# Optimization experiments

Measured on AMD Instinct MI355X. Metric: run time of the kernel, lower is better.

The kernel has to match this reference:

```python
import jax, jax.numpy as jnp
import numpy as np

N = 50000      # nodes
E = 800000     # edges (before self-loops)
IN = 64        # in_dim
C = 64         # hidden_dim (per-head out channels)
H = 4          # heads
NEG_SLOPE = 0.2


def setup_inputs() -> dict:
    key = jax.random.key(0)
    ks = jax.random.split(key, 9)
    x = jax.random.normal(ks[0], (N, IN), jnp.float32)
    edge_index = jax.random.randint(ks[1], (2, E), 0, N)
    edge_attr = jax.random.uniform(ks[2], (E, 1), jnp.float32)
    s_in = 1.0 / np.sqrt(IN)
    s_c = 1.0 / np.sqrt(C)
    W = jax.random.normal(ks[3], (IN, H * C), jnp.float32) * s_in
    att_src = jax.random.normal(ks[4], (H, C), jnp.float32) * s_c
    att_dst = jax.random.normal(ks[5], (H, C), jnp.float32) * s_c
    lin_edge_w = jax.random.normal(ks[6], (1, H * C), jnp.float32)
    att_edge = jax.random.normal(ks[7], (H, C), jnp.float32) * s_c
    bias = jnp.zeros((C,), jnp.float32)
    return dict(x=x, edge_index=edge_index, edge_attr=edge_attr, W=W,
                att_src=att_src, att_dst=att_dst, lin_edge_w=lin_edge_w,
                att_edge=att_edge, bias=bias)


def reference(x, edge_index, edge_attr, W, att_src, att_dst, lin_edge_w, att_edge, bias):
    n = x.shape[0]
    # add self-loops (PyG default add_self_loops=True, fill_value='mean')
    loop = jnp.arange(n)
    src = jnp.concatenate([edge_index[0], loop])          # [E+N]
    dst = jnp.concatenate([edge_index[1], loop])          # [E+N]
    ea = jnp.concatenate([edge_attr,
                          jnp.full((n, 1), edge_attr.mean(), edge_attr.dtype)], axis=0)
    # node transform: [N, H, C]
    h = (x @ W).reshape(n, H, C)
    a_src = jnp.einsum('nhc,hc->nh', h, att_src)          # [N, H]
    a_dst = jnp.einsum('nhc,hc->nh', h, att_dst)          # [N, H]
    eh = (ea @ lin_edge_w).reshape(-1, H, C)              # [E+N, H, C]
    a_edge = jnp.einsum('ehc,hc->eh', eh, att_edge)       # [E+N, H]
    # per-edge attention logit
    alpha = a_src[src] + a_dst[dst] + a_edge              # [E+N, H]
    alpha = jax.nn.leaky_relu(alpha, NEG_SLOPE)
    # segment softmax over edges grouped by destination node
    amax = jax.ops.segment_max(alpha, dst, num_segments=n)
    alpha = jnp.exp(alpha - amax[dst])
    asum = jax.ops.segment_sum(alpha, dst, num_segments=n)
    alpha = alpha / (asum[dst] + 1e-16)                   # [E+N, H]
    # weighted message + scatter-add aggregation
    msg = h[src] * alpha[..., None]                       # [E+N, H, C]
    out = jax.ops.segment_sum(msg, dst, num_segments=n)   # [N, H, C]
    out = out.mean(axis=1) + bias                         # concat=False -> head mean
    # ReLU + residual
    return jax.nn.relu(out) + x
```

## Files before the change

### kernel.cpp

```cpp
#include <hip/hip_runtime.h>
#include <hip/hip_fp16.h>
#include <math.h>

#define H 4
#define C 64
#define HC 256
#define NEG 0.2f
#define ROWU 64
#define MAXREC 63
#define XPAD 72
#define HPAD 264
#define BKT 128
#define BSH 7
#define TILE 2048
#define SEG 32
#define SEGSH 5

typedef __attribute__((ext_vector_type(8))) _Float16 half8;
typedef __attribute__((ext_vector_type(4))) float f32x4;
typedef float f32x2 __attribute__((vector_size(8)));

__global__ __launch_bounds__(256) void phase1_kernel(
    const float* __restrict__ x, const float* __restrict__ W,
    const float* __restrict__ att_src, const float* __restrict__ att_dst,
    const int* __restrict__ ei, const float* __restrict__ edge_attr,
    unsigned char* __restrict__ h, float* __restrict__ a_src, float* __restrict__ a_dst,
    uint2* __restrict__ arena, unsigned* __restrict__ counts,
    float* __restrict__ mean_acc, int Nn, int Ee, int G1, int ntile) {
    int t = threadIdx.x;
    if ((int)blockIdx.x < G1) {
        __shared__ __align__(16) _Float16 xs[16 * XPAD];
        __shared__ __align__(16) _Float16 hs[16 * HPAD];
        int w = t >> 6, lane = t & 63, quad = lane >> 4, c16 = lane & 15;
        half8 bf[4][2];
#pragma unroll
        for (int nt = 0; nt < 4; ++nt)
#pragma unroll
            for (int kh = 0; kh < 2; ++kh)
#pragma unroll
                for (int j = 0; j < 8; ++j)
                    bf[nt][kh][j] = (_Float16)W[(kh * 32 + quad * 8 + j) * HC +
                                                w * 64 + nt * 16 + c16];
        float ats[4], atd[4];
#pragma unroll
        for (int nt = 0; nt < 4; ++nt) {
            ats[nt] = att_src[w * 64 + nt * 16 + c16];
            atd[nt] = att_dst[w * 64 + nt * 16 + c16];
        }

        int nTiles = (Nn + 15) >> 4;
        for (int mt = blockIdx.x; mt < nTiles; mt += G1) {
            __syncthreads();
            {
                int row = t >> 4, col4 = (t & 15) * 4;
                int node = mt * 16 + row;
                float4 v = make_float4(0.f, 0.f, 0.f, 0.f);
                if (node < Nn) v = *(const float4*)(x + (size_t)node * 64 + col4);
                _Float16* dst = xs + row * XPAD + col4;
                dst[0] = (_Float16)v.x; dst[1] = (_Float16)v.y;
                dst[2] = (_Float16)v.z; dst[3] = (_Float16)v.w;
            }
            __syncthreads();
            half8 a0 = *(const half8*)(xs + c16 * XPAD + quad * 8);
            half8 a1 = *(const half8*)(xs + c16 * XPAD + 32 + quad * 8);
            f32x4 d[4];
#pragma unroll
            for (int nt = 0; nt < 4; ++nt) {
                f32x4 acc = {0.f, 0.f, 0.f, 0.f};
                acc = __builtin_amdgcn_mfma_f32_16x16x32_f16(a0, bf[nt][0], acc, 0, 0, 0);
                acc = __builtin_amdgcn_mfma_f32_16x16x32_f16(a1, bf[nt][1], acc, 0, 0, 0);
                d[nt] = acc;
            }
#pragma unroll
            for (int reg = 0; reg < 4; ++reg) {
                float ps = 0.f, pd = 0.f;
#pragma unroll
                for (int nt = 0; nt < 4; ++nt) {
                    ps += d[nt][reg] * ats[nt];
                    pd += d[nt][reg] * atd[nt];
                }
                ps += __shfl_xor(ps, 1); pd += __shfl_xor(pd, 1);
                ps += __shfl_xor(ps, 2); pd += __shfl_xor(pd, 2);
                ps += __shfl_xor(ps, 4); pd += __shfl_xor(pd, 4);
                ps += __shfl_xor(ps, 8); pd += __shfl_xor(pd, 8);
                if (c16 == 0) {
                    int node = mt * 16 + quad * 4 + reg;
                    if (node < Nn) {
                        a_src[node * 4 + w] = ps;
                        a_dst[node * 4 + w] = pd;
                    }
                }
            }
#pragma unroll
            for (int nt = 0; nt < 4; ++nt)
#pragma unroll
                for (int reg = 0; reg < 4; ++reg)
                    hs[(quad * 4 + reg) * HPAD + w * 64 + nt * 16 + c16] =
                        (_Float16)d[nt][reg];
            __syncthreads();
            {
                int row = t >> 4, chunk = t & 15;
                int node = mt * 16 + row;
                if (node < Nn) {
                    const uint4* sp = (const uint4*)(hs + row * HPAD + chunk * 16);
                    uint4 sA = sp[0], sB = sp[1];
                    unsigned ua[8] = {sA.x, sA.y, sA.z, sA.w, sB.x, sB.y, sB.z, sB.w};
                    unsigned ow[4];
#pragma unroll
                    for (int q = 0; q < 4; ++q) {
                        float2 p0 = __half22float2(*reinterpret_cast<const __half2*>(&ua[q * 2]));
                        float2 p1 = __half22float2(*reinterpret_cast<const __half2*>(&ua[q * 2 + 1]));
                        int v = __builtin_amdgcn_cvt_pk_fp8_f32(p0.x, p0.y, 0, false);
                        v = __builtin_amdgcn_cvt_pk_fp8_f32(p1.x, p1.y, v, true);
                        ow[q] = (unsigned)v;
                    }
                    *(uint4*)(h + (size_t)node * HC + chunk * 16) =
                        make_uint4(ow[0], ow[1], ow[2], ow[3]);
                }
            }
        }
    } else {
        __shared__ float red[256];
        __shared__ unsigned cntA[512];
        int nbkt = (Nn + BKT - 1) >> BSH;
        int tile = (int)blockIdx.x - G1;
        for (int bb = t; bb < nbkt; bb += 256) cntA[bb] = 0;
        __syncthreads();
        int e0 = tile * TILE;
        float s = 0.f;
#pragma unroll 4
        for (int k = 0; k < TILE / 256; ++k) {
            int i = e0 + k * 256 + t;
            if (i < Ee) {
                int src = ei[i];
                int dst = ei[Ee + i];
                float ea = edge_attr[i];
                s += ea;
                unsigned q = (unsigned)(ea * 65535.f + 0.5f);
                int b = dst >> BSH;
                unsigned r = atomicAdd(&cntA[b], 1u);
                if (r < SEG)
                    arena[((size_t)b * ntile + tile) * SEG + r] =
                        make_uint2((q << 16) | (unsigned)src,
                                   (unsigned)(dst & (BKT - 1)));
            }
        }
        __syncthreads();
        for (int bb = t; bb < nbkt; bb += 256) {
            unsigned c = cntA[bb];
            counts[(size_t)bb * ntile + tile] = c < (unsigned)SEG ? c : (unsigned)SEG;
        }
        red[t] = s;
        __syncthreads();
        for (int o = 128; o; o >>= 1) {
            if (t < o) red[t] += red[t + o];
            __syncthreads();
        }
        if (t == 0) atomicAdd(mean_acc, red[0]);
    }
}

__global__ __launch_bounds__(256) void bucket_kernel(
    const uint2* __restrict__ arena, const unsigned* __restrict__ counts,
    unsigned* __restrict__ edges, int ntile) {
    __shared__ unsigned rows[BKT * ROWU];
    __shared__ unsigned cnt[BKT];
    __shared__ unsigned short segc[512];
    int b = blockIdx.x, t = threadIdx.x;
    if (t < BKT) cnt[t] = 0;
    for (int j = t; j < ntile; j += 256)
        segc[j] = (unsigned short)counts[(size_t)b * ntile + j];
    __syncthreads();
    int total = ntile * SEG;
    size_t base = (size_t)b * ntile * SEG;
    for (int j = t; j < total; j += 256) {
        int seg = j >> SEGSH, slot = j & (SEG - 1);
        if (slot < (int)segc[seg]) {
            uint2 e = arena[base + j];
            unsigned r = atomicAdd(&cnt[e.y], 1u);
            if (r < MAXREC) rows[e.y * ROWU + 1 + r] = e.x;
        }
    }
    __syncthreads();
    if (t < BKT) rows[t * ROWU] = cnt[t] < (unsigned)MAXREC ? cnt[t] : (unsigned)MAXREC;
    __syncthreads();
    size_t obase = (size_t)b * (BKT * ROWU);
    for (int i = t; i < BKT * (ROWU / 4); i += 256)
        *(uint4*)(edges + obase + i * 4) = *(const uint4*)(rows + i * 4);
}

__global__ __launch_bounds__(256) void aggregate_kernel(
    const unsigned* __restrict__ edges,
    const float* __restrict__ a_src, const float* __restrict__ a_dst,
    const float* __restrict__ lin_edge_w, const float* __restrict__ att_edge,
    const float* __restrict__ mean_acc, const unsigned char* __restrict__ h,
    const float* __restrict__ bias, const float* __restrict__ x,
    float* __restrict__ out, int Nn, float invE) {
    int lane = threadIdx.x & 63;
    int n = blockIdx.x * 4 + (threadIdx.x >> 6);
    if (n >= Nn) return;
    int head = lane >> 4;

    size_t rowbase = (size_t)n * ROWU;
    unsigned deg = edges[rowbase];
    unsigned rec = edges[rowbase + 1 + lane];
    const unsigned* h8 = (const unsigned*)h;
    unsigned sv = h8[(size_t)n * 64 + lane];
    float mean = mean_acc[0] * invE;
    float ad = a_dst[n * 4 + head];
    float asn = a_src[n * 4 + head];

    int sub = lane & 15;
    float kp = 0.f;
#pragma unroll
    for (int j = 0; j < 4; ++j) {
        int c = sub * 4 + j;
        kp += lin_edge_w[head * C + c] * att_edge[head * C + c];
    }
    kp += __shfl_xor(kp, 1);
    kp += __shfl_xor(kp, 2);
    kp += __shfl_xor(kp, 4);
    kp += __shfl_xor(kp, 8);
    float K = kp;
    const float DEQ = 1.0f / 65535.f;

    if (deg > MAXREC) deg = MAXREC;

    float ls = asn + ad + mean * K;
    ls = ls > 0.f ? ls : NEG * ls;
    float wsl = __expf(ls);
    f32x2 s01 = __builtin_amdgcn_cvt_pk_f32_fp8((int)sv, false);
    f32x2 s23 = __builtin_amdgcn_cvt_pk_f32_fp8((int)sv, true);
    float4 acc = make_float4(wsl * s01[0], wsl * s01[1], wsl * s23[0], wsl * s23[1]);
    float swgt = wsl;

    int i = 0;
    for (; i + 4 <= (int)deg; i += 4) {
        unsigned r0 = (unsigned)__builtin_amdgcn_readlane((int)rec, i + 0);
        unsigned r1 = (unsigned)__builtin_amdgcn_readlane((int)rec, i + 1);
        unsigned r2 = (unsigned)__builtin_amdgcn_readlane((int)rec, i + 2);
        unsigned r3 = (unsigned)__builtin_amdgcn_readlane((int)rec, i + 3);
        int s0 = r0 & 0xFFFF, s1 = r1 & 0xFFFF, s2 = r2 & 0xFFFF, s3 = r3 & 0xFFFF;
        unsigned hv0 = h8[(size_t)s0 * 64 + lane];
        unsigned hv1 = h8[(size_t)s1 * 64 + lane];
        unsigned hv2 = h8[(size_t)s2 * 64 + lane];
        unsigned hv3 = h8[(size_t)s3 * 64 + lane];
        float l0 = a_src[s0 * 4 + head] + ad + (float)(r0 >> 16) * DEQ * K;
        float l1 = a_src[s1 * 4 + head] + ad + (float)(r1 >> 16) * DEQ * K;
        float l2 = a_src[s2 * 4 + head] + ad + (float)(r2 >> 16) * DEQ * K;
        float l3 = a_src[s3 * 4 + head] + ad + (float)(r3 >> 16) * DEQ * K;
        l0 = l0 > 0.f ? l0 : NEG * l0;
        l1 = l1 > 0.f ? l1 : NEG * l1;
        l2 = l2 > 0.f ? l2 : NEG * l2;
        l3 = l3 > 0.f ? l3 : NEG * l3;
        float w0 = __expf(l0), w1 = __expf(l1), w2 = __expf(l2), w3 = __expf(l3);
        swgt += (w0 + w1) + (w2 + w3);
        {
            f32x2 f01 = __builtin_amdgcn_cvt_pk_f32_fp8((int)hv0, false);
            f32x2 f23 = __builtin_amdgcn_cvt_pk_f32_fp8((int)hv0, true);
            acc.x += w0 * f01[0]; acc.y += w0 * f01[1];
            acc.z += w0 * f23[0]; acc.w += w0 * f23[1];
        }
        {
            f32x2 f01 = __builtin_amdgcn_cvt_pk_f32_fp8((int)hv1, false);
            f32x2 f23 = __builtin_amdgcn_cvt_pk_f32_fp8((int)hv1, true);
            acc.x += w1 * f01[0]; acc.y += w1 * f01[1];
            acc.z += w1 * f23[0]; acc.w += w1 * f23[1];
        }
        {
            f32x2 f01 = __builtin_amdgcn_cvt_pk_f32_fp8((int)hv2, false);
            f32x2 f23 = __builtin_amdgcn_cvt_pk_f32_fp8((int)hv2, true);
            acc.x += w2 * f01[0]; acc.y += w2 * f01[1];
            acc.z += w2 * f23[0]; acc.w += w2 * f23[1];
        }
        {
            f32x2 f01 = __builtin_amdgcn_cvt_pk_f32_fp8((int)hv3, false);
            f32x2 f23 = __builtin_amdgcn_cvt_pk_f32_fp8((int)hv3, true);
            acc.x += w3 * f01[0]; acc.y += w3 * f01[1];
            acc.z += w3 * f23[0]; acc.w += w3 * f23[1];
        }
    }
    for (; i < (int)deg; ++i) {
        unsigned r = (unsigned)__builtin_amdgcn_readlane((int)rec, i);
        int s0 = r & 0xFFFF;
        unsigned hv = h8[(size_t)s0 * 64 + lane];
        float l = a_src[s0 * 4 + head] + ad + (float)(r >> 16) * DEQ * K;
        l = l > 0.f ? l : NEG * l;
        float wg = __expf(l);
        swgt += wg;
        f32x2 f01 = __builtin_amdgcn_cvt_pk_f32_fp8((int)hv, false);
        f32x2 f23 = __builtin_amdgcn_cvt_pk_f32_fp8((int)hv, true);
        acc.x += wg * f01[0]; acc.y += wg * f01[1];
        acc.z += wg * f23[0]; acc.w += wg * f23[1];
    }

    float inv = 1.f / (swgt + 1e-16f);
    acc.x *= inv; acc.y *= inv; acc.z *= inv; acc.w *= inv;

    acc.x += __shfl_xor(acc.x, 16);
    acc.y += __shfl_xor(acc.y, 16);
    acc.z += __shfl_xor(acc.z, 16);
    acc.w += __shfl_xor(acc.w, 16);
    acc.x += __shfl_xor(acc.x, 32);
    acc.y += __shfl_xor(acc.y, 32);
    acc.z += __shfl_xor(acc.z, 32);
    acc.w += __shfl_xor(acc.w, 32);
    if (lane < 16) {
        float4 b = ((const float4*)bias)[lane];
        float4 xv = ((const float4*)x)[(size_t)n * 16 + lane];
        float4 o;
        o.x = fmaxf(acc.x * 0.25f + b.x, 0.f) + xv.x;
        o.y = fmaxf(acc.y * 0.25f + b.y, 0.f) + xv.y;
        o.z = fmaxf(acc.z * 0.25f + b.z, 0.f) + xv.z;
        o.w = fmaxf(acc.w * 0.25f + b.w, 0.f) + xv.w;
        ((float4*)out)[(size_t)n * 16 + lane] = o;
    }
}

extern "C" void kernel_launch(void* const* d_in, const int* in_sizes, int n_in,
                              void* d_out, int out_size, void* d_ws, size_t ws_size,
                              hipStream_t stream) {
    const float* x = (const float*)d_in[0];
    const int* ei = (const int*)d_in[1];
    const float* edge_attr = (const float*)d_in[2];
    const float* W = (const float*)d_in[3];
    const float* att_src = (const float*)d_in[4];
    const float* att_dst = (const float*)d_in[5];
    const float* lin_edge_w = (const float*)d_in[6];
    const float* att_edge = (const float*)d_in[7];
    const float* bias = (const float*)d_in[8];
    float* out = (float*)d_out;
    int Nn = in_sizes[0] / 64;
    int Ee = in_sizes[1] / 2;
    int NB = (Nn + BKT - 1) >> BSH;
    int ntile = (Ee + TILE - 1) / TILE;

    char* p = (char*)d_ws;
    size_t off = 0;
    auto alloc = [&](size_t bytes) -> char* {
        char* r = p + off;
        off += (bytes + 255) & ~(size_t)255;
        return r;
    };
    float* mean_acc = (float*)alloc(256);
    size_t zero_bytes = off;
    unsigned* counts = (unsigned*)alloc((size_t)NB * ntile * 4);
    uint2* arena = (uint2*)alloc((size_t)NB * ntile * SEG * 8);
    unsigned* edges = (unsigned*)alloc((size_t)NB * BKT * ROWU * 4);
    unsigned char* h = (unsigned char*)alloc((size_t)Nn * HC);
    float* a_src = (float*)alloc((size_t)Nn * H * 4);
    float* a_dst = (float*)alloc((size_t)Nn * H * 4);
    (void)ws_size;

    const int G1 = 512;
    hipMemsetAsync(d_ws, 0, zero_bytes, stream);
    phase1_kernel<<<G1 + ntile, 256, 0, stream>>>(x, W, att_src, att_dst, ei, edge_attr,
                                                  h, a_src, a_dst, arena, counts,
                                                  mean_acc, Nn, Ee, G1, ntile);
    bucket_kernel<<<NB, 256, 0, stream>>>(arena, counts, edges, ntile);
    aggregate_kernel<<<(Nn + 3) / 4, 256, 0, stream>>>(edges, a_src, a_dst,
                                                       lin_edge_w, att_edge, mean_acc,
                                                       h, bias, x, out, Nn,
                                                       1.0f / (float)Ee);
}
```

Measured before the change: 164.1 us.

## Transpose arena layout to tile-major and precompute edge weights in parallel

```diff
diff --git a/kernel.cpp b/kernel.cpp
--- a/kernel.cpp
+++ b/kernel.cpp
@@ -127,6 +127,7 @@
         for (int bb = t; bb < nbkt; bb += 256) cntA[bb] = 0;
         __syncthreads();
         int e0 = tile * TILE;
+        size_t tbase = (size_t)tile * nbkt;
         float s = 0.f;
 #pragma unroll 4
         for (int k = 0; k < TILE / 256; ++k) {
@@ -140,7 +141,7 @@
                 int b = dst >> BSH;
                 unsigned r = atomicAdd(&cntA[b], 1u);
                 if (r < SEG)
-                    arena[((size_t)b * ntile + tile) * SEG + r] =
+                    arena[(tbase + b) * SEG + r] =
                         make_uint2((q << 16) | (unsigned)src,
                                    (unsigned)(dst & (BKT - 1)));
             }
@@ -148,7 +149,7 @@
         __syncthreads();
         for (int bb = t; bb < nbkt; bb += 256) {
             unsigned c = cntA[bb];
-            counts[(size_t)bb * ntile + tile] = c < (unsigned)SEG ? c : (unsigned)SEG;
+            counts[tbase + bb] = c < (unsigned)SEG ? c : (unsigned)SEG;
         }
         red[t] = s;
         __syncthreads();
@@ -162,21 +163,20 @@
 
 __global__ __launch_bounds__(256) void bucket_kernel(
     const uint2* __restrict__ arena, const unsigned* __restrict__ counts,
-    unsigned* __restrict__ edges, int ntile) {
+    unsigned* __restrict__ edges, int ntile, int nbkt) {
     __shared__ unsigned rows[BKT * ROWU];
     __shared__ unsigned cnt[BKT];
     __shared__ unsigned short segc[512];
     int b = blockIdx.x, t = threadIdx.x;
     if (t < BKT) cnt[t] = 0;
     for (int j = t; j < ntile; j += 256)
-        segc[j] = (unsigned short)counts[(size_t)b * ntile + j];
+        segc[j] = (unsigned short)counts[(size_t)j * nbkt + b];
     __syncthreads();
     int total = ntile * SEG;
-    size_t base = (size_t)b * ntile * SEG;
     for (int j = t; j < total; j += 256) {
         int seg = j >> SEGSH, slot = j & (SEG - 1);
         if (slot < (int)segc[seg]) {
-            uint2 e = arena[base + j];
+            uint2 e = arena[((size_t)seg * nbkt + b) * SEG + slot];
             unsigned r = atomicAdd(&cnt[e.y], 1u);
             if (r < MAXREC) rows[e.y * ROWU + 1 + r] = e.x;
         }
@@ -200,6 +200,7 @@
     int n = blockIdx.x * 4 + (threadIdx.x >> 6);
     if (n >= Nn) return;
     int head = lane >> 4;
+    int sub = lane & 15;
 
     size_t rowbase = (size_t)n * ROWU;
     unsigned deg = edges[rowbase];
@@ -210,7 +211,6 @@
     float ad = a_dst[n * 4 + head];
     float asn = a_src[n * 4 + head];
 
-    int sub = lane & 15;
     float kp = 0.f;
 #pragma unroll
     for (int j = 0; j < 4; ++j) {
@@ -226,72 +226,91 @@
 
     if (deg > MAXREC) deg = MAXREC;
 
+    float wk0, wk1, wk2, wk3;
+    {
+        float wtmp[4];
+#pragma unroll
+        for (int k = 0; k < 4; ++k) {
+            int e = sub + 16 * k;
+            unsigned re = (unsigned)__shfl((int)rec, e);
+            int se = (e < (int)deg) ? (int)(re & 0xFFFF) : 0;
+            float lg = a_src[se * 4 + head] + ad + (float)(re >> 16) * DEQ * K;
+            lg = lg > 0.f ? lg : NEG * lg;
+            wtmp[k] = (e < (int)deg) ? __expf(lg) : 0.f;
+        }
+        wk0 = wtmp[0]; wk1 = wtmp[1]; wk2 = wtmp[2]; wk3 = wtmp[3];
+    }
+    float sw = (wk0 + wk1) + (wk2 + wk3);
+    sw += __shfl_xor(sw, 1);
+    sw += __shfl_xor(sw, 2);
+    sw += __shfl_xor(sw, 4);
+    sw += __shfl_xor(sw, 8);
+
     float ls = asn + ad + mean * K;
     ls = ls > 0.f ? ls : NEG * ls;
     float wsl = __expf(ls);
     f32x2 s01 = __builtin_amdgcn_cvt_pk_f32_fp8((int)sv, false);
     f32x2 s23 = __builtin_amdgcn_cvt_pk_f32_fp8((int)sv, true);
     float4 acc = make_float4(wsl * s01[0], wsl * s01[1], wsl * s23[0], wsl * s23[1]);
-    float swgt = wsl;
-
-    int i = 0;
-    for (; i + 4 <= (int)deg; i += 4) {
-        unsigned r0 = (unsigned)__builtin_amdgcn_readlane((int)rec, i + 0);
-        unsigned r1 = (unsigned)__builtin_amdgcn_readlane((int)rec, i + 1);
-        unsigned r2 = (unsigned)__builtin_amdgcn_readlane((int)rec, i + 2);
-        unsigned r3 = (unsigned)__builtin_amdgcn_readlane((int)rec, i + 3);
-        int s0 = r0 & 0xFFFF, s1 = r1 & 0xFFFF, s2 = r2 & 0xFFFF, s3 = r3 & 0xFFFF;
-        unsigned hv0 = h8[(size_t)s0 * 64 + lane];
-        unsigned hv1 = h8[(size_t)s1 * 64 + lane];
-        unsigned hv2 = h8[(size_t)s2 * 64 + lane];
-        unsigned hv3 = h8[(size_t)s3 * 64 + lane];
-        float l0 = a_src[s0 * 4 + head] + ad + (float)(r0 >> 16) * DEQ * K;
-        float l1 = a_src[s1 * 4 + head] + ad + (float)(r1 >> 16) * DEQ * K;
-        float l2 = a_src[s2 * 4 + head] + ad + (float)(r2 >> 16) * DEQ * K;
-        float l3 = a_src[s3 * 4 + head] + ad + (float)(r3 >> 16) * DEQ * K;
-        l0 = l0 > 0.f ? l0 : NEG * l0;
-        l1 = l1 > 0.f ? l1 : NEG * l1;
-        l2 = l2 > 0.f ? l2 : NEG * l2;
-        l3 = l3 > 0.f ? l3 : NEG * l3;
-        float w0 = __expf(l0), w1 = __expf(l1), w2 = __expf(l2), w3 = __expf(l3);
-        swgt += (w0 + w1) + (w2 + w3);
-        {
-            f32x2 f01 = __builtin_amdgcn_cvt_pk_f32_fp8((int)hv0, false);
-            f32x2 f23 = __builtin_amdgcn_cvt_pk_f32_fp8((int)hv0, true);
-            acc.x += w0 * f01[0]; acc.y += w0 * f01[1];
-            acc.z += w0 * f23[0]; acc.w += w0 * f23[1];
-        }
-        {
-            f32x2 f01 = __builtin_amdgcn_cvt_pk_f32_fp8((int)hv1, false);
-            f32x2 f23 = __builtin_amdgcn_cvt_pk_f32_fp8((int)hv1, true);
-            acc.x += w1 * f01[0]; acc.y += w1 * f01[1];
-            acc.z += w1 * f23[0]; acc.w += w1 * f23[1];
-        }
-        {
-            f32x2 f01 = __builtin_amdgcn_cvt_pk_f32_fp8((int)hv2, false);
-            f32x2 f23 = __builtin_amdgcn_cvt_pk_f32_fp8((int)hv2, true);
-            acc.x += w2 * f01[0]; acc.y += w2 * f01[1];
-            acc.z += w2 * f23[0]; acc.w += w2 * f23[1];
-        }
-        {
-            f32x2 f01 = __builtin_amdgcn_cvt_pk_f32_fp8((int)hv3, false);
-            f32x2 f23 = __builtin_amdgcn_cvt_pk_f32_fp8((int)hv3, true);
-            acc.x += w3 * f01[0]; acc.y += w3 * f01[1];
-            acc.z += w3 * f23[0]; acc.w += w3 * f23[1];
-        }
-    }
-    for (; i < (int)deg; ++i) {
-        unsigned r = (unsigned)__builtin_amdgcn_readlane((int)rec, i);
-        int s0 = r & 0xFFFF;
-        unsigned hv = h8[(size_t)s0 * 64 + lane];
-        float l = a_src[s0 * 4 + head] + ad + (float)(r >> 16) * DEQ * K;
-        l = l > 0.f ? l : NEG * l;
-        float wg = __expf(l);
-        swgt += wg;
-        f32x2 f01 = __builtin_amdgcn_cvt_pk_f32_fp8((int)hv, false);
-        f32x2 f23 = __builtin_amdgcn_cvt_pk_f32_fp8((int)hv, true);
-        acc.x += wg * f01[0]; acc.y += wg * f01[1];
-        acc.z += wg * f23[0]; acc.w += wg * f23[1];
+    float swgt = sw + wsl;
+    int hb = lane & 48;
+
+#pragma unroll
+    for (int k = 0; k < 4; ++k) {
+        int base = k * 16;
+        if (base >= (int)deg) break;
+        float wsrc = (k == 0) ? wk0 : (k == 1) ? wk1 : (k == 2) ? wk2 : wk3;
+        int cnt = (int)deg - base;
+        if (cnt > 16) cnt = 16;
+        int j = 0;
+        for (; j + 4 <= cnt; j += 4) {
+            int e0 = base + j;
+            unsigned r0 = (unsigned)__builtin_amdgcn_readlane((int)rec, e0 + 0);
+            unsigned r1 = (unsigned)__builtin_amdgcn_readlane((int)rec, e0 + 1);
+            unsigned r2 = (unsigned)__builtin_amdgcn_readlane((int)rec, e0 + 2);
+            unsigned r3 = (unsigned)__builtin_amdgcn_readlane((int)rec, e0 + 3);
+            unsigned hv0 = h8[(size_t)(r0 & 0xFFFF) * 64 + lane];
+            unsigned hv1 = h8[(size_t)(r1 & 0xFFFF) * 64 + lane];
+            unsigned hv2 = h8[(size_t)(r2 & 0xFFFF) * 64 + lane];
+            unsigned hv3 = h8[(size_t)(r3 & 0xFFFF) * 64 + lane];
+            float w0 = __shfl(wsrc, hb | (j + 0));
+            float w1 = __shfl(wsrc, hb | (j + 1));
+            float w2 = __shfl(wsrc, hb | (j + 2));
+            float w3 = __shfl(wsrc, hb | (j + 3));
+            {
+                f32x2 f01 = __builtin_amdgcn_cvt_pk_f32_fp8((int)hv0, false);
+                f32x2 f23 = __builtin_amdgcn_cvt_pk_f32_fp8((int)hv0, true);
+                acc.x += w0 * f01[0]; acc.y += w0 * f01[1];
+                acc.z += w0 * f23[0]; acc.w += w0 * f23[1];
+            }
+            {
+                f32x2 f01 = __builtin_amdgcn_cvt_pk_f32_fp8((int)hv1, false);
+                f32x2 f23 = __builtin_amdgcn_cvt_pk_f32_fp8((int)hv1, true);
+                acc.x += w1 * f01[0]; acc.y += w1 * f01[1];
+                acc.z += w1 * f23[0]; acc.w += w1 * f23[1];
+            }
+            {
+                f32x2 f01 = __builtin_amdgcn_cvt_pk_f32_fp8((int)hv2, false);
+                f32x2 f23 = __builtin_amdgcn_cvt_pk_f32_fp8((int)hv2, true);
+                acc.x += w2 * f01[0]; acc.y += w2 * f01[1];
+                acc.z += w2 * f23[0]; acc.w += w2 * f23[1];
+            }
+            {
+                f32x2 f01 = __builtin_amdgcn_cvt_pk_f32_fp8((int)hv3, false);
+                f32x2 f23 = __builtin_amdgcn_cvt_pk_f32_fp8((int)hv3, true);
+                acc.x += w3 * f01[0]; acc.y += w3 * f01[1];
+                acc.z += w3 * f23[0]; acc.w += w3 * f23[1];
+            }
+        }
+        for (; j < cnt; ++j) {
+            unsigned r = (unsigned)__builtin_amdgcn_readlane((int)rec, base + j);
+            unsigned hv = h8[(size_t)(r & 0xFFFF) * 64 + lane];
+            float wg = __shfl(wsrc, hb | j);
+            f32x2 f01 = __builtin_amdgcn_cvt_pk_f32_fp8((int)hv, false);
+            f32x2 f23 = __builtin_amdgcn_cvt_pk_f32_fp8((int)hv, true);
+            acc.x += wg * f01[0]; acc.y += wg * f01[1];
+            acc.z += wg * f23[0]; acc.w += wg * f23[1];
+        }
     }
 
     float inv = 1.f / (swgt + 1e-16f);
@@ -344,8 +363,8 @@
     };
     float* mean_acc = (float*)alloc(256);
     size_t zero_bytes = off;
-    unsigned* counts = (unsigned*)alloc((size_t)NB * ntile * 4);
-    uint2* arena = (uint2*)alloc((size_t)NB * ntile * SEG * 8);
+    unsigned* counts = (unsigned*)alloc((size_t)ntile * NB * 4);
+    uint2* arena = (uint2*)alloc((size_t)ntile * NB * SEG * 8);
     unsigned* edges = (unsigned*)alloc((size_t)NB * BKT * ROWU * 4);
     unsigned char* h = (unsigned char*)alloc((size_t)Nn * HC);
     float* a_src = (float*)alloc((size_t)Nn * H * 4);
@@ -357,7 +376,7 @@
     phase1_kernel<<<G1 + ntile, 256, 0, stream>>>(x, W, att_src, att_dst, ei, edge_attr,
                                                   h, a_src, a_dst, arena, counts,
                                                   mean_acc, Nn, Ee, G1, ntile);
-    bucket_kernel<<<NB, 256, 0, stream>>>(arena, counts, edges, ntile);
+    bucket_kernel<<<NB, 256, 0, stream>>>(arena, counts, edges, ntile, NB);
     aggregate_kernel<<<(Nn + 3) / 4, 256, 0, stream>>>(edges, a_src, a_dst,
                                                        lin_edge_w, att_edge, mean_acc,
                                                        h, bias, x, out, Nn,
```

New measurement: 161.9 us. No clear change (-1.3%).
